# Optimization experiments

Hardware: AMD Instinct MI355X
Metric: run time of the kernel (lower is better)

Reference implementation:

```python
import jax, jax.numpy as jnp
import numpy as np

B = 64          # decode batch (num_tokens, q_len=1 each)
HIDDEN = 4096
NH = 32         # query heads
NKV = 8         # kv heads (GQA)
HD = 128        # head_dim = hidden/NH
S = 2048        # max cached context per sequence
BLOCK = 16      # paged-cache block size
NBLK = B * (S // BLOCK)  # 8192 physical blocks
THETA = 10000.0


def _rope(x, positions):
    # x: [B, H, D] -- neox-style (half-split) llama RoPE
    d = x.shape[-1]
    inv_freq = 1.0 / (THETA ** (jnp.arange(0, d, 2, dtype=jnp.float32) / d))  # [D/2]
    ang = positions.astype(jnp.float32)[:, None] * inv_freq[None, :]          # [B, D/2]
    cos = jnp.cos(ang)[:, None, :]
    sin = jnp.sin(ang)[:, None, :]
    x1, x2 = jnp.split(x, 2, axis=-1)
    return jnp.concatenate([x1 * cos - x2 * sin, x2 * cos + x1 * sin], axis=-1)


def setup_inputs() -> dict:
    key = jax.random.key(0)
    ks = jax.random.split(key, 10)
    hidden_states = jax.random.randint(ks[0], (B, HIDDEN), -128, 128, dtype=jnp.int32).astype(jnp.int8)
    w_qkv = jax.random.randint(ks[1], (HIDDEN, (NH + 2 * NKV) * HD), -128, 128, dtype=jnp.int32).astype(jnp.int8)
    w_o = jax.random.randint(ks[2], (NH * HD, HIDDEN), -128, 128, dtype=jnp.int32).astype(jnp.int8)
    k_cache = jax.random.randint(ks[3], (NBLK, BLOCK, NKV, HD), -128, 128, dtype=jnp.int32).astype(jnp.int8)
    v_cache = jax.random.randint(ks[4], (NBLK, BLOCK, NKV, HD), -128, 128, dtype=jnp.int32).astype(jnp.int8)
    block_tables = jnp.arange(NBLK, dtype=jnp.int32).reshape(B, S // BLOCK)
    context_lens = jax.random.randint(ks[5], (B,), 256, S, dtype=jnp.int32)
    positions = context_lens  # new token appended at index context_len
    q_scale = jax.random.uniform(ks[6], (), minval=0.005, maxval=0.02, dtype=jnp.float32)
    k_scale = jax.random.uniform(ks[7], (), minval=0.005, maxval=0.02, dtype=jnp.float32)
    v_scale = jax.random.uniform(ks[8], (), minval=0.005, maxval=0.02, dtype=jnp.float32)
    o_scale = jax.random.uniform(ks[9], (), minval=0.005, maxval=0.02, dtype=jnp.float32)
    return dict(positions=positions, hidden_states=hidden_states, w_qkv=w_qkv, w_o=w_o,
                k_cache=k_cache, v_cache=v_cache, block_tables=block_tables,
                context_lens=context_lens, q_scale=q_scale, k_scale=k_scale,
                v_scale=v_scale, o_scale=o_scale)


def reference(positions, hidden_states, w_qkv, w_o, k_cache, v_cache,
              block_tables, context_lens, q_scale, k_scale, v_scale, o_scale):
    scaling = HD ** -0.5
    q_size, kv_size = NH * HD, NKV * HD
    qkv = jnp.matmul(hidden_states.astype(jnp.int32), w_qkv.astype(jnp.int32))  # [B, 6144]
    # fused dequant + RoPE
    q = qkv[:, :q_size].astype(jnp.float32).reshape(B, NH, HD) * q_scale
    k = qkv[:, q_size:q_size + kv_size].astype(jnp.float32).reshape(B, NKV, HD) * k_scale
    v = qkv[:, q_size + kv_size:].astype(jnp.float32).reshape(B, NKV, HD) * v_scale
    q = _rope(q, positions)
    k = _rope(k, positions)
    # paged-cache gather + dequant: [B, n_blk, BLOCK, NKV, HD] -> [B, S, NKV, HD]
    K = (k_cache[block_tables].astype(jnp.float32) * k_scale).reshape(B, S, NKV, HD)
    V = (v_cache[block_tables].astype(jnp.float32) * v_scale).reshape(B, S, NKV, HD)
    # append current token's k/v (as the cache write would)
    K = jnp.concatenate([K, k[:, None]], axis=1)  # [B, S+1, NKV, HD]
    V = jnp.concatenate([V, v[:, None]], axis=1)
    idx = jnp.arange(S + 1)
    valid = (idx[None, :] < context_lens[:, None]) | (idx[None, :] == S)  # [B, S+1]
    # GQA: group query heads over kv heads
    qg = q.reshape(B, NKV, NH // NKV, HD)
    scores = jnp.einsum('bhgd,bshd->bhgs', qg, K) * scaling  # [B, NKV, G, S+1]
    scores = jnp.where(valid[:, None, None, :], scores, jnp.float32(-1e30))
    p = jax.nn.softmax(scores, axis=-1)
    attn = jnp.einsum('bhgs,bshd->bhgd', p, V).reshape(B, NH * HD)
    # quantized o_proj with dequant scale
    out = jnp.matmul(attn, w_o.astype(jnp.float32)) * o_scale  # [B, HIDDEN]
    return out
```

## Files before the change

### kernel.cpp

```cpp
#include <hip/hip_runtime.h>

typedef int   v4i  __attribute__((ext_vector_type(4)));
typedef short bf8  __attribute__((ext_vector_type(8)));
typedef float f32x4 __attribute__((ext_vector_type(4)));

#define B_   64
#define HIDDEN_ 4096
#define NH_  32
#define NKV_ 8
#define HD_  128
#define S_   2048
#define NQKV 6144
#define CHUNK 256
#define NCHUNK 8
#define KSPLIT 8
#define QKV_PART (64 * NQKV)

__device__ __forceinline__ unsigned pack_i8(int a, int b, int c, int d) {
    return (a & 0xff) | ((b & 0xff) << 8) | ((c & 0xff) << 16) | (d << 24);
}

__global__ __launch_bounds__(256) void qkv_gemm(const int* __restrict__ A,
                                                const int* __restrict__ W,
                                                int* __restrict__ Cp) {
    __shared__ signed char Wl[2][64 * 80];
    const int tid = threadIdx.x;
    const int n0  = blockIdx.x * 64;
    const int ky  = blockIdx.y;
    const int kbeg = ky * (HIDDEN_ / KSPLIT);
    const int wv  = tid >> 6;
    const int l   = tid & 63;
    const int lr  = l & 15;
    const int lk  = l >> 4;
    const int sn  = tid & 63;
    const int sk  = (tid >> 6) * 16;

    const int* Wg = W + (long)(kbeg + sk) * NQKV + n0 + sn;

    v4i acc[4] = {v4i{0,0,0,0}, v4i{0,0,0,0}, v4i{0,0,0,0}, v4i{0,0,0,0}};
    int rA[16], rB[16];

#define LOADW(R, CH) { const int* wp = Wg + (long)(CH) * 64 * NQKV;              \
    _Pragma("unroll") for (int j = 0; j < 16; ++j) R[j] = wp[j * NQKV]; }
#define STAGEW(R, BUF) { unsigned d0 = pack_i8(R[0],R[1],R[2],R[3]);             \
    unsigned d1 = pack_i8(R[4],R[5],R[6],R[7]);                                  \
    unsigned d2 = pack_i8(R[8],R[9],R[10],R[11]);                                \
    unsigned d3 = pack_i8(R[12],R[13],R[14],R[15]);                              \
    v4i t = {(int)d0,(int)d1,(int)d2,(int)d3};                                   \
    *(v4i*)&Wl[BUF][sn * 80 + sk] = t; }
#define COMPW(BUF, CH) { const int* ap = A + (long)(wv*16+lr)*HIDDEN_ + kbeg + (CH)*64 + lk*16; \
    unsigned av[4];                                                              \
    _Pragma("unroll") for (int j = 0; j < 4; ++j) {                              \
        int4 t = *(const int4*)(ap + 4*j); av[j] = pack_i8(t.x,t.y,t.z,t.w); }   \
    v4i a = *(v4i*)av;                                                           \
    _Pragma("unroll") for (int nt = 0; nt < 4; ++nt) {                           \
        v4i bb = *(const v4i*)&Wl[BUF][(nt*16+lr)*80 + lk*16];                   \
        acc[nt] = __builtin_amdgcn_mfma_i32_16x16x64_i8(a, bb, acc[nt], 0,0,0); } }

    LOADW(rA, 0);
#pragma unroll 1
    for (int ch = 0; ch < 8; ch += 2) {
        STAGEW(rA, 0);
        LOADW(rB, ch + 1);
        __syncthreads();
        COMPW(0, ch);
        STAGEW(rB, 1);
        if (ch < 6) LOADW(rA, ch + 2);
        __syncthreads();
        COMPW(1, ch + 1);
    }
    int* Co = Cp + (long)ky * QKV_PART;
#pragma unroll
    for (int nt = 0; nt < 4; ++nt)
#pragma unroll
        for (int r = 0; r < 4; ++r) {
            int m = wv * 16 + (l >> 4) * 4 + r;
            int n = n0 + nt * 16 + (l & 15);
            Co[m * NQKV + n] = acc[nt][r];
        }
#undef LOADW
#undef STAGEW
#undef COMPW
}

__device__ __forceinline__ float rd8(const int* __restrict__ q, int idx) {
    int v = 0;
#pragma unroll
    for (int p = 0; p < KSPLIT; ++p) v += q[p * QKV_PART + idx];
    return (float)v;
}

__global__ __launch_bounds__(256) void rope_dequant(const int* __restrict__ qkvp,
                                                    const int* __restrict__ positions,
                                                    const float* qs_p, const float* ks_p,
                                                    const float* vs_p,
                                                    float* __restrict__ qf,
                                                    float* __restrict__ knew,
                                                    float* __restrict__ vnew) {
    const int b = blockIdx.x, part = blockIdx.y;
    const int tid = threadIdx.x;
    __shared__ float cs[64], sn[64];
    const float qs = qs_p[0], ks = ks_p[0], vs = vs_p[0];
    if (tid < 64) {
        float invf = 1.0f / powf(10000.0f, (float)tid * (1.0f / 64.0f));
        float ang  = (float)positions[b] * invf;
        cs[tid] = cosf(ang);
        sn[tid] = sinf(ang);
    }
    __syncthreads();
    const int base = b * NQKV;
    if (part < 2) {
        for (int t = tid; t < 1024; t += 256) {
            int head = part * 16 + (t >> 6), i = t & 63;
            float x1 = rd8(qkvp, base + head * 128 + i) * qs;
            float x2 = rd8(qkvp, base + head * 128 + 64 + i) * qs;
            float c = cs[i], s = sn[i];
            qf[(b * NH_ + head) * 128 + i]      = x1 * c - x2 * s;
            qf[(b * NH_ + head) * 128 + 64 + i] = x2 * c + x1 * s;
        }
    } else if (part == 2) {
        for (int t = tid; t < 512; t += 256) {
            int h = t >> 6, i = t & 63;
            float x1 = rd8(qkvp, base + 4096 + h * 128 + i) * ks;
            float x2 = rd8(qkvp, base + 4096 + h * 128 + 64 + i) * ks;
            float c = cs[i], s = sn[i];
            knew[(b * NKV_ + h) * 128 + i]      = x1 * c - x2 * s;
            knew[(b * NKV_ + h) * 128 + 64 + i] = x2 * c + x1 * s;
        }
    } else {
        for (int t = tid; t < 1024; t += 256) {
            int h = t >> 7, d = t & 127;
            vnew[(b * NKV_ + h) * 128 + d] = rd8(qkvp, base + 5120 + h * 128 + d) * vs;
        }
    }
}

__global__ __launch_bounds__(256, 4) void attn_decode(const int* __restrict__ kc,
                                                      const int* __restrict__ vc,
                                                      const int* __restrict__ btab,
                                                      const int* __restrict__ ctx_lens,
                                                      const float* __restrict__ qf,
                                                      const float* ks_p, const float* vs_p,
                                                      float* __restrict__ po,
                                                      float* __restrict__ pm,
                                                      float* __restrict__ pl) {
    const int c  = blockIdx.x;
    const int bh = blockIdx.y;
    const int b = bh >> 3, h = bh & 7;
    const int ctx = ctx_lens[b];
    const int s0g = c * CHUNK;
    const int n = min(ctx - s0g, CHUNK);
    if (n <= 0) return;

    __shared__ float sc[4][264];
    __shared__ float opart[512][9];
    __shared__ int   bts[CHUNK / 16];

    const int tid = threadIdx.x;
    const int wv  = tid >> 6;
    const int l   = tid & 63;
    const int tok = l >> 4;
    const int dq  = l & 15;

    if (tid < CHUNK / 16) bts[tid] = btab[b * 128 + (s0g >> 4) + tid];

    const float kss = ks_p[0] * 0.08838834764831845f;
    const float vscale = vs_p[0];

    float qr[4][8];
#pragma unroll
    for (int g = 0; g < 4; ++g) {
        const float* qp = qf + (long)(b * NH_ + h * 4 + g) * 128 + dq * 8;
        float4 v0 = *(const float4*)(qp);
        float4 v1 = *(const float4*)(qp + 4);
        qr[g][0]=v0.x; qr[g][1]=v0.y; qr[g][2]=v0.z; qr[g][3]=v0.w;
        qr[g][4]=v1.x; qr[g][5]=v1.y; qr[g][6]=v1.z; qr[g][7]=v1.w;
    }
    __syncthreads();

    {
        const int nsweep = (n + 15) >> 4;
        int srel = wv * 4 + tok;
        int4 w0, w1;
        {
            int seff = min(srel, n - 1);
            int blk = bts[seff >> 4];
            const int* kp = kc + (long)(blk * 16 + (seff & 15)) * 1024 + h * 128 + dq * 8;
            w0 = *(const int4*)kp;
            w1 = *(const int4*)(kp + 4);
        }
#pragma unroll 1
        for (int it = 0; it < nsweep; ++it) {
            int4 u0, u1;
            const bool more = (it + 1 < nsweep);
            if (more) {
                int snx = min(srel + 16, n - 1);
                int blk = bts[snx >> 4];
                const int* kp = kc + (long)(blk * 16 + (snx & 15)) * 1024 + h * 128 + dq * 8;
                u0 = *(const int4*)kp;
                u1 = *(const int4*)(kp + 4);
            }
            float kf[8];
            kf[0]=(float)w0.x; kf[1]=(float)w0.y; kf[2]=(float)w0.z; kf[3]=(float)w0.w;
            kf[4]=(float)w1.x; kf[5]=(float)w1.y; kf[6]=(float)w1.z; kf[7]=(float)w1.w;
            float p0 = 0.f, p1 = 0.f, p2 = 0.f, p3 = 0.f;
#pragma unroll
            for (int j = 0; j < 8; ++j) {
                p0 += qr[0][j] * kf[j];
                p1 += qr[1][j] * kf[j];
                p2 += qr[2][j] * kf[j];
                p3 += qr[3][j] * kf[j];
            }
#pragma unroll
            for (int off = 1; off < 16; off <<= 1) {
                p0 += __shfl_xor(p0, off, 16);
                p1 += __shfl_xor(p1, off, 16);
                p2 += __shfl_xor(p2, off, 16);
                p3 += __shfl_xor(p3, off, 16);
            }
            if (srel < n && dq < 4) {
                float psel = (dq == 0) ? p0 : (dq == 1) ? p1 : (dq == 2) ? p2 : p3;
                sc[dq][srel] = psel * kss;
            }
            if (more) { w0 = u0; w1 = u1; }
            srel += 16;
        }
    }
    __syncthreads();

    {
        float m = -1e30f;
        for (int s = l; s < n; s += 64) m = fmaxf(m, sc[wv][s]);
#pragma unroll
        for (int off = 1; off < 64; off <<= 1) m = fmaxf(m, __shfl_xor(m, off, 64));
        float sum = 0.f;
        for (int s = l; s < n; s += 64) {
            float e = __expf(sc[wv][s] - m);
            sc[wv][s] = e;
            sum += e;
        }
#pragma unroll
        for (int off = 1; off < 64; off <<= 1) sum += __shfl_xor(sum, off, 64);
        if (l == 0) {
            int idx = (c * 512 + bh) * 4 + wv;
            pm[idx] = m;
            pl[idx] = sum;
        }
    }
    __syncthreads();

    const int d4 = tid & 31;
    const int sp = tid >> 5;
    float acc[4][4] = {};
    int s = sp;
#pragma unroll 1
    for (; s + 56 < n; s += 64) {
        int4 w[8];
#pragma unroll
        for (int j = 0; j < 8; ++j) {
            int ss = s + 8 * j;
            int blk = bts[ss >> 4];
            w[j] = *(const int4*)(vc + (long)(blk * 16 + (ss & 15)) * 1024 + h * 128 + d4 * 4);
        }
#pragma unroll
        for (int j = 0; j < 8; ++j) {
            int ss = s + 8 * j;
            float v0 = (float)w[j].x, v1 = (float)w[j].y, v2 = (float)w[j].z, v3 = (float)w[j].w;
#pragma unroll
            for (int g = 0; g < 4; ++g) {
                float p = sc[g][ss];
                acc[g][0] += p * v0; acc[g][1] += p * v1;
                acc[g][2] += p * v2; acc[g][3] += p * v3;
            }
        }
    }
#pragma unroll 1
    for (; s < n; s += 8) {
        int blk = bts[s >> 4];
        int4 w = *(const int4*)(vc + (long)(blk * 16 + (s & 15)) * 1024 + h * 128 + d4 * 4);
        float v0 = (float)w.x, v1 = (float)w.y, v2 = (float)w.z, v3 = (float)w.w;
#pragma unroll
        for (int g = 0; g < 4; ++g) {
            float p = sc[g][s];
            acc[g][0] += p * v0; acc[g][1] += p * v1;
            acc[g][2] += p * v2; acc[g][3] += p * v3;
        }
    }
#pragma unroll
    for (int g = 0; g < 4; ++g)
#pragma unroll
        for (int j = 0; j < 4; ++j)
            opart[g * 128 + d4 * 4 + j][sp] = acc[g][j];
    __syncthreads();

    for (int oi = tid; oi < 512; oi += 256) {
        float o = 0.f;
#pragma unroll
        for (int p = 0; p < 8; ++p) o += opart[oi][p];
        po[(long)((c * 512 + bh) * 4 + (oi >> 7)) * 128 + (oi & 127)] = o * vscale;
    }
}

__global__ __launch_bounds__(256) void attn_merge(const float* __restrict__ qf,
                                                  const float* __restrict__ knew,
                                                  const float* __restrict__ vnew,
                                                  const int* __restrict__ ctx_lens,
                                                  const float* __restrict__ po,
                                                  const float* __restrict__ pm,
                                                  const float* __restrict__ pl,
                                                  unsigned short* __restrict__ attn) {
    const int bh = blockIdx.x;
    const int b = bh >> 3, h = bh & 7;
    const int ctx = ctx_lens[b];
    const int nc = (ctx + CHUNK - 1) / CHUNK;
    const int tid = threadIdx.x;
    const int wv = tid >> 6, l = tid & 63;
    __shared__ float snew_s[4];

    {
        const float* kn = knew + (b * NKV_ + h) * 128;
        const float* qp = qf + (long)(b * NH_ + h * 4 + wv) * 128;
        float p = qp[l] * kn[l] + qp[l + 64] * kn[l + 64];
#pragma unroll
        for (int off = 1; off < 64; off <<= 1) p += __shfl_xor(p, off, 64);
        if (l == 0) snew_s[wv] = p * 0.08838834764831845f;
    }
    __syncthreads();

    for (int oi = tid; oi < 512; oi += 256) {
        int g = oi >> 7, d = oi & 127;
        float snew = snew_s[g];
        float M = snew;
        float mc[NCHUNK];
        for (int c = 0; c < nc; ++c) {
            mc[c] = pm[(c * 512 + bh) * 4 + g];
            M = fmaxf(M, mc[c]);
        }
        float wn = __expf(snew - M);
        float L = wn;
        float O = wn * vnew[(b * NKV_ + h) * 128 + d];
        for (int c = 0; c < nc; ++c) {
            float w = __expf(mc[c] - M);
            L += pl[(c * 512 + bh) * 4 + g] * w;
            O += po[(long)((c * 512 + bh) * 4 + g) * 128 + d] * w;
        }
        float res = O / L;
        unsigned int u = __float_as_uint(res);
        unsigned int r = (u + 0x7fffu + ((u >> 16) & 1u)) >> 16;
        attn[b * 4096 + (h * 4 + g) * 128 + d] = (unsigned short)r;
    }
}

__global__ __launch_bounds__(256) void oproj(const unsigned short* __restrict__ Abf,
                                             const int* __restrict__ W,
                                             const float* os_p,
                                             float* __restrict__ out) {
    __shared__ unsigned short Wl[4][16 * 72];
    const int tid = threadIdx.x;
    const int n0  = blockIdx.x * 16;
    const int wv  = tid >> 6, l = tid & 63;
    const int lr  = l & 15, lk = l >> 4;
    const float osc = os_p[0];
    const int sn  = tid & 15;
    const int sk4 = (tid >> 4) * 4;

    const int* Wg = W + (long)sk4 * HIDDEN_ + n0 + sn;

    f32x4 acc = f32x4{0.f, 0.f, 0.f, 0.f};
    int r0[4], r1[4], r2[4], r3[4];

#define LOADO(R, CH) { const int* wp = Wg + (long)(CH) * 64 * HIDDEN_;           \
    _Pragma("unroll") for (int j = 0; j < 4; ++j) R[j] = wp[j * HIDDEN_]; }
#define STAGEO(R, BUF) { ushort4 hb;                                             \
    hb.x = (unsigned short)(__float_as_uint((float)R[0]) >> 16);                 \
    hb.y = (unsigned short)(__float_as_uint((float)R[1]) >> 16);                 \
    hb.z = (unsigned short)(__float_as_uint((float)R[2]) >> 16);                 \
    hb.w = (unsigned short)(__float_as_uint((float)R[3]) >> 16);                 \
    *(ushort4*)&Wl[BUF][sn * 72 + sk4] = hb; }
#define COMPO(BUF, CH) { _Pragma("unroll") for (int kh = 0; kh < 2; ++kh) {      \
    bf8 a = *(const bf8*)(Abf + (long)(wv*16+lr)*HIDDEN_ + (CH)*64 + kh*32 + lk*8); \
    bf8 bb = *(const bf8*)&Wl[BUF][lr * 72 + kh * 32 + lk * 8];                  \
    acc = __builtin_amdgcn_mfma_f32_16x16x32_bf16(a, bb, acc, 0, 0, 0); } }

    LOADO(r0, 0); LOADO(r1, 1); LOADO(r2, 2); LOADO(r3, 3);
#pragma unroll 1
    for (int ch = 0; ch < 64; ch += 4) {
        STAGEO(r0, 0); STAGEO(r1, 1); STAGEO(r2, 2); STAGEO(r3, 3);
        __syncthreads();
        if (ch < 60) { LOADO(r0, ch+4); LOADO(r1, ch+5); LOADO(r2, ch+6); LOADO(r3, ch+7); }
        COMPO(0, ch); COMPO(1, ch+1); COMPO(2, ch+2); COMPO(3, ch+3);
        __syncthreads();
    }
#pragma unroll
    for (int r = 0; r < 4; ++r) {
        int m = wv * 16 + (l >> 4) * 4 + r;
        int n = n0 + (l & 15);
        out[m * HIDDEN_ + n] = acc[r] * osc;
    }
#undef LOADO
#undef STAGEO
#undef COMPO
}

extern "C" void kernel_launch(void* const* d_in, const int* in_sizes, int n_in,
                              void* d_out, int out_size, void* d_ws, size_t ws_size,
                              hipStream_t stream) {
    const int*   positions = (const int*)d_in[0];
    const int*   hidden    = (const int*)d_in[1];
    const int*   w_qkv     = (const int*)d_in[2];
    const int*   w_o       = (const int*)d_in[3];
    const int*   kcache    = (const int*)d_in[4];
    const int*   vcache    = (const int*)d_in[5];
    const int*   btab      = (const int*)d_in[6];
    const int*   ctxl      = (const int*)d_in[7];
    const float* qs        = (const float*)d_in[8];
    const float* ks        = (const float*)d_in[9];
    const float* vs        = (const float*)d_in[10];
    const float* os        = (const float*)d_in[11];

    char* ws = (char*)d_ws;
    int*            qkvp  = (int*)ws;
    float*          qf    = (float*)(ws + 12582912);
    float*          knew  = (float*)(ws + 13631488);
    float*          vnew  = (float*)(ws + 13893632);
    unsigned short* attnb = (unsigned short*)(ws + 14155776);
    float*          po    = (float*)(ws + 14680064);
    float*          pm    = (float*)(ws + 23068672);
    float*          pl    = (float*)(ws + 23134208);

    qkv_gemm<<<dim3(NQKV / 64, KSPLIT), 256, 0, stream>>>(hidden, w_qkv, qkvp);
    rope_dequant<<<dim3(B_, 4), 256, 0, stream>>>(qkvp, positions, qs, ks, vs, qf, knew, vnew);
    attn_decode<<<dim3(NCHUNK, B_ * NKV_), 256, 0, stream>>>(kcache, vcache, btab, ctxl,
                                                             qf, ks, vs, po, pm, pl);
    attn_merge<<<B_ * NKV_, 256, 0, stream>>>(qf, knew, vnew, ctxl, po, pm, pl, attnb);
    oproj<<<HIDDEN_ / 16, 256, 0, stream>>>(attnb, w_o, os, (float*)d_out);
}
```

Measured before the change: 234.9 us.

## Halve attention chunk size and restructure PV loop to per-wave heads

Halves the split-K attention chunk to 128 tokens, doubling the number of chunks and blocks in the decode grid. The P·V stage now gives each wave one query head and each lane two head dims, iterating over all tokens. This removes the shared-memory cross-partition reduction and its extra barrier. The workspace is relaid so the larger partial-output buffer overlaps the qkv partial buffer, which is dead by then. The cost is narrower 8-byte V loads, each V row fetched four times (once per head wave), and twice the merge work.

Measured after the change: 321.9 us. 37.0% more time.

```diff
diff --git a/kernel.cpp b/kernel.cpp
--- a/kernel.cpp
+++ b/kernel.cpp
@@ -11,8 +11,8 @@
 #define HD_  128
 #define S_   2048
 #define NQKV 6144
-#define CHUNK 256
-#define NCHUNK 8
+#define CHUNK 128
+#define NCHUNK 16
 #define KSPLIT 8
 #define QKV_PART (64 * NQKV)
 
@@ -135,15 +135,15 @@
     }
 }
 
-__global__ __launch_bounds__(256, 4) void attn_decode(const int* __restrict__ kc,
-                                                      const int* __restrict__ vc,
-                                                      const int* __restrict__ btab,
-                                                      const int* __restrict__ ctx_lens,
-                                                      const float* __restrict__ qf,
-                                                      const float* ks_p, const float* vs_p,
-                                                      float* __restrict__ po,
-                                                      float* __restrict__ pm,
-                                                      float* __restrict__ pl) {
+__global__ __launch_bounds__(256) void attn_decode(const int* __restrict__ kc,
+                                                   const int* __restrict__ vc,
+                                                   const int* __restrict__ btab,
+                                                   const int* __restrict__ ctx_lens,
+                                                   const float* __restrict__ qf,
+                                                   const float* ks_p, const float* vs_p,
+                                                   float* __restrict__ po,
+                                                   float* __restrict__ pm,
+                                                   float* __restrict__ pl) {
     const int c  = blockIdx.x;
     const int bh = blockIdx.y;
     const int b = bh >> 3, h = bh & 7;
@@ -152,8 +152,7 @@
     const int n = min(ctx - s0g, CHUNK);
     if (n <= 0) return;
 
-    __shared__ float sc[4][264];
-    __shared__ float opart[512][9];
+    __shared__ float sc[4][132];
     __shared__ int   bts[CHUNK / 16];
 
     const int tid = threadIdx.x;
@@ -249,55 +248,39 @@
     }
     __syncthreads();
 
-    const int d4 = tid & 31;
-    const int sp = tid >> 5;
-    float acc[4][4] = {};
-    int s = sp;
-#pragma unroll 1
-    for (; s + 56 < n; s += 64) {
-        int4 w[8];
-#pragma unroll
-        for (int j = 0; j < 8; ++j) {
-            int ss = s + 8 * j;
-            int blk = bts[ss >> 4];
-            w[j] = *(const int4*)(vc + (long)(blk * 16 + (ss & 15)) * 1024 + h * 128 + d4 * 4);
-        }
-#pragma unroll
-        for (int j = 0; j < 8; ++j) {
-            int ss = s + 8 * j;
-            float v0 = (float)w[j].x, v1 = (float)w[j].y, v2 = (float)w[j].z, v3 = (float)w[j].w;
-#pragma unroll
-            for (int g = 0; g < 4; ++g) {
-                float p = sc[g][ss];
-                acc[g][0] += p * v0; acc[g][1] += p * v1;
-                acc[g][2] += p * v2; acc[g][3] += p * v3;
-            }
-        }
-    }
-#pragma unroll 1
-    for (; s < n; s += 8) {
-        int blk = bts[s >> 4];
-        int4 w = *(const int4*)(vc + (long)(blk * 16 + (s & 15)) * 1024 + h * 128 + d4 * 4);
-        float v0 = (float)w.x, v1 = (float)w.y, v2 = (float)w.z, v3 = (float)w.w;
-#pragma unroll
-        for (int g = 0; g < 4; ++g) {
+    {
+        const int g  = wv;
+        const int dp = l;
+        const int* vbase = vc + h * 128 + dp * 2;
+        float a0 = 0.f, a1 = 0.f;
+        int s = 0;
+#pragma unroll 1
+        for (; s + 7 < n; s += 8) {
+            int2 w[8];
+#pragma unroll
+            for (int j = 0; j < 8; ++j) {
+                int ss = s + j;
+                int blk = bts[ss >> 4];
+                w[j] = *(const int2*)(vbase + (long)(blk * 16 + (ss & 15)) * 1024);
+            }
+#pragma unroll
+            for (int j = 0; j < 8; ++j) {
+                float p = sc[g][s + j];
+                a0 += p * (float)w[j].x;
+                a1 += p * (float)w[j].y;
+            }
+        }
+#pragma unroll 1
+        for (; s < n; ++s) {
+            int blk = bts[s >> 4];
+            int2 w = *(const int2*)(vbase + (long)(blk * 16 + (s & 15)) * 1024);
             float p = sc[g][s];
-            acc[g][0] += p * v0; acc[g][1] += p * v1;
-            acc[g][2] += p * v2; acc[g][3] += p * v3;
-        }
-    }
-#pragma unroll
-    for (int g = 0; g < 4; ++g)
-#pragma unroll
-        for (int j = 0; j < 4; ++j)
-            opart[g * 128 + d4 * 4 + j][sp] = acc[g][j];
-    __syncthreads();
-
-    for (int oi = tid; oi < 512; oi += 256) {
-        float o = 0.f;
-#pragma unroll
-        for (int p = 0; p < 8; ++p) o += opart[oi][p];
-        po[(long)((c * 512 + bh) * 4 + (oi >> 7)) * 128 + (oi & 127)] = o * vscale;
+            a0 += p * (float)w.x;
+            a1 += p * (float)w.y;
+        }
+        float* op = po + (long)((c * 512 + bh) * 4 + g) * 128 + dp * 2;
+        op[0] = a0 * vscale;
+        op[1] = a1 * vscale;
     }
 }
 
@@ -332,6 +315,7 @@
         float snew = snew_s[g];
         float M = snew;
         float mc[NCHUNK];
+#pragma unroll 1
         for (int c = 0; c < nc; ++c) {
             mc[c] = pm[(c * 512 + bh) * 4 + g];
             M = fmaxf(M, mc[c]);
@@ -339,6 +323,7 @@
         float wn = __expf(snew - M);
         float L = wn;
         float O = wn * vnew[(b * NKV_ + h) * 128 + d];
+#pragma unroll 1
         for (int c = 0; c < nc; ++c) {
             float w = __expf(mc[c] - M);
             L += pl[(c * 512 + bh) * 4 + g] * w;
@@ -420,13 +405,13 @@
 
     char* ws = (char*)d_ws;
     int*            qkvp  = (int*)ws;
-    float*          qf    = (float*)(ws + 12582912);
-    float*          knew  = (float*)(ws + 13631488);
-    float*          vnew  = (float*)(ws + 13893632);
-    unsigned short* attnb = (unsigned short*)(ws + 14155776);
-    float*          po    = (float*)(ws + 14680064);
-    float*          pm    = (float*)(ws + 23068672);
-    float*          pl    = (float*)(ws + 23134208);
+    float*          po    = (float*)ws;
+    float*          qf    = (float*)(ws + 16777216);
+    float*          knew  = (float*)(ws + 17825792);
+    float*          vnew  = (float*)(ws + 18087936);
+    unsigned short* attnb = (unsigned short*)(ws + 18350080);
+    float*          pm    = (float*)(ws + 18874368);
+    float*          pl    = (float*)(ws + 19005440);
 
     qkv_gemm<<<dim3(NQKV / 64, KSPLIT), 256, 0, stream>>>(hidden, w_qkv, qkvp);
     rope_dequant<<<dim3(B_, 4), 256, 0, stream>>>(qkvp, positions, qs, ks, vs, qf, knew, vnew);
```
